# Kernel optimization log

Measured on AMD Instinct MI355X. Metric: run time of the kernel, lower is better.

## Reference

```python
import jax, jax.numpy as jnp
import numpy as np
from math import sqrt

LOCAL_WINDOW = 32
STRIDE = 64


def _sparse_mask(L):
    # L_Q == L_K path of DozerAttention:
    #  - local window: diagonals at offsets 0..local_window//2 (both signs)
    #  - strided: diagonals at offsets 0, stride+1, 2*(stride+1), ... (both signs)
    i = jnp.arange(L)[:, None]
    j = jnp.arange(L)[None, :]
    d = jnp.abs(i - j)
    local = d <= (LOCAL_WINDOW // 2)
    strided = (d % (STRIDE + 1)) == 0
    return (local | strided).astype(jnp.float32)  # [L, L]


def setup_inputs() -> dict:
    key = jax.random.key(0)
    B, L, H, D = 2, 2048, 8, 64
    kq, kk, kv = jax.random.split(key, 3)
    queries = jax.random.normal(kq, (B, L, H, D), dtype=jnp.float32)
    keys = jax.random.normal(kk, (B, L, H, D), dtype=jnp.float32)
    values = jax.random.normal(kv, (B, L, H, D), dtype=jnp.float32)
    # TriangularCausalMask: True above the diagonal -> masked with -inf
    causal = jnp.triu(jnp.ones((L, L), dtype=bool), k=1)
    attn_mask = jnp.broadcast_to(causal[None, None], (B, 1, L, L))
    return {"queries": queries, "keys": keys, "values": values, "attn_mask": attn_mask}


def reference(queries, keys, values, attn_mask):
    B, L, H, D = queries.shape
    scale = 1.0 / sqrt(D)
    sm = _sparse_mask(L)  # [L, L]
    # Original fills a zero-initialized dense score tensor only at selected key
    # columns per query row; equivalent to dense QK^T elementwise-masked by sm
    # (non-selected entries stay exactly 0, NOT -inf -- faithful quirk).
    scores = jnp.einsum('blhe,bshe->bhls', queries, keys) * sm  # [B,H,L,L]
    scores = jnp.where(attn_mask, -jnp.inf, scores)
    A = jax.nn.softmax(scale * scores, axis=-1)  # dropout p=0.0 in this config
    V = jnp.einsum('bhls,bshd->blhd', A, values)  # [B,L,H,D]
    return V
```

## Files before the change

kernel.cpp:

```cpp
#include <hip/hip_runtime.h>
#include <hip/hip_bf16.h>

#define B_ 2
#define L_ 2048
#define H_ 8
#define D_ 64
#define SP_ 65
#define NC_ 128
#define NL2_ 8
#define RS_ 512

typedef __attribute__((ext_vector_type(8))) short bf16x8;
typedef __attribute__((ext_vector_type(16))) float f32x16;

static __device__ inline short f2bf(float x) {
    return __builtin_bit_cast(short, __float2bfloat16(x));
}

static __device__ inline bf16x8 ld8_bf16(const float* __restrict__ p) {
    float4 a = *(const float4*)p;
    float4 b = *(const float4*)(p + 4);
    bf16x8 r;
    r[0]=f2bf(a.x); r[1]=f2bf(a.y); r[2]=f2bf(a.z); r[3]=f2bf(a.w);
    r[4]=f2bf(b.x); r[5]=f2bf(b.y); r[6]=f2bf(b.z); r[7]=f2bf(b.w);
    return r;
}

static __device__ inline bf16x8 ones_frag() {
    bf16x8 r;
    short o = f2bf(1.f);
    #pragma unroll
    for (int t = 0; t < 8; ++t) r[t] = o;
    return r;
}

__global__ __launch_bounds__(256) void partials_k(const float* __restrict__ q,
                                                  const float* __restrict__ kk,
                                                  const float* __restrict__ v,
                                                  float* __restrict__ csum1,
                                                  float* __restrict__ csum2,
                                                  float* __restrict__ pA,
                                                  float* __restrict__ zA,
                                                  float* __restrict__ pB,
                                                  float* __restrict__ zB) {
    __shared__ float Pw[4][32][68];
    int wib  = threadIdx.x >> 6;
    int lane = threadIdx.x & 63;
    int half = lane >> 5, ln = lane & 31;
    int u = blockIdx.x * 4 + wib;

    if (u < 1024) {
        int bh = u >> 6;
        int T  = (u & 63) << 5;
        int h = bh & 7, b = bh >> 3;
        const size_t base = (size_t)b * L_ * RS_ + (size_t)h * D_;

        bf16x8 bv0[4], bv1[4];
        #pragma unroll
        for (int kb = 0; kb < 4; ++kb) {
            int k0 = kb * 16 + half * 8;
            #pragma unroll
            for (int jj = 0; jj < 8; ++jj) {
                int jr = T - 16 + k0 + jj;
                jr = jr < 0 ? 0 : (jr > L_ - 1 ? L_ - 1 : jr);
                const float* vr = v + base + (size_t)jr * RS_;
                bv0[kb][jj] = f2bf(vr[ln]);
                bv1[kb][jj] = f2bf(vr[32 + ln]);
            }
        }

        const float* qrow = q + base + (size_t)(T + ln) * RS_;
        bf16x8 aq[4];
        #pragma unroll
        for (int kb = 0; kb < 4; ++kb) aq[kb] = ld8_bf16(qrow + kb * 16 + half * 8);

        int j0 = T - 16 + ln; j0 = j0 < 0 ? 0 : j0;
        int j1 = T + 16 + ln; j1 = j1 > L_ - 1 ? L_ - 1 : j1;
        const float* kr0 = kk + base + (size_t)j0 * RS_;
        const float* kr1 = kk + base + (size_t)j1 * RS_;
        f32x16 acc0 = {}; f32x16 acc1 = {};
        #pragma unroll
        for (int kb = 0; kb < 4; ++kb) {
            bf16x8 b0 = ld8_bf16(kr0 + kb * 16 + half * 8);
            bf16x8 b1 = ld8_bf16(kr1 + kb * 16 + half * 8);
            acc0 = __builtin_amdgcn_mfma_f32_32x32x16_bf16(aq[kb], b0, acc0, 0, 0, 0);
            acc1 = __builtin_amdgcn_mfma_f32_32x32x16_bf16(aq[kb], b1, acc1, 0, 0, 0);
        }

        #pragma unroll
        for (int r = 0; r < 16; ++r) {
            int m = (r & 3) + 8 * (r >> 2) + 4 * half;
            bool a0 = (ln >= m) && (ln <= m + 16) && (T - 16 + ln >= 0);
            float w0 = a0 ? (__expf(0.125f * acc0[r]) - 1.f) : 0.f;
            if ((m < 16) && (ln >= 16) && (ln <= m + 16)) w0 += 1.f;
            bool a1 = (ln <= m - 16);
            float w1 = a1 ? (__expf(0.125f * acc1[r]) - 1.f) : 0.f;
            if ((m >= 16) && (ln <= m - 16)) w1 += 1.f;
            Pw[wib][m][ln]      = w0;
            Pw[wib][m][32 + ln] = w1;
        }
        __syncthreads();

        f32x16 p0 = {}; f32x16 p1 = {}; f32x16 po = {};
        bf16x8 ones = ones_frag();
        #pragma unroll
        for (int kb = 0; kb < 4; ++kb) {
            int k0 = kb * 16 + half * 8;
            const float* pr = &Pw[wib][ln][k0];
            float4 x = *(const float4*)pr;
            float4 y = *(const float4*)(pr + 4);
            bf16x8 ap;
            ap[0]=f2bf(x.x); ap[1]=f2bf(x.y); ap[2]=f2bf(x.z); ap[3]=f2bf(x.w);
            ap[4]=f2bf(y.x); ap[5]=f2bf(y.y); ap[6]=f2bf(y.z); ap[7]=f2bf(y.w);
            p0 = __builtin_amdgcn_mfma_f32_32x32x16_bf16(ap, bv0[kb], p0, 0, 0, 0);
            p1 = __builtin_amdgcn_mfma_f32_32x32x16_bf16(ap, bv1[kb], p1, 0, 0, 0);
            po = __builtin_amdgcn_mfma_f32_32x32x16_bf16(ap, ones,    po, 0, 0, 0);
        }

        float* pAr = pA + (size_t)bh * L_ * D_;
        float* zAr = zA + (size_t)bh * L_;
        #pragma unroll
        for (int r = 0; r < 16; ++r) {
            int m = (r & 3) + 8 * (r >> 2) + 4 * half;
            int i = T + m;
            pAr[(size_t)i * D_ + ln]      = p0[r];
            pAr[(size_t)i * D_ + 32 + ln] = p1[r];
            if (ln == 0) zAr[i] = po[r] - (float)((m & 15) + 1);
        }
    } else if (u < 2064) {
        int us = u - 1024;
        int bh = us / SP_;
        int r  = us % SP_;
        int h = bh & 7, b = bh >> 3;
        const size_t base = (size_t)b * L_ * RS_ + (size_t)h * D_;

        bf16x8 bv0[2], bv1[2];
        #pragma unroll
        for (int kb = 0; kb < 2; ++kb) {
            int k0 = kb * 16 + half * 8;
            #pragma unroll
            for (int jj = 0; jj < 8; ++jj) {
                int lv = r + SP_ * (k0 + jj);
                lv = lv > L_ - 1 ? L_ - 1 : lv;
                const float* vr = v + base + (size_t)lv * RS_;
                bv0[kb][jj] = f2bf(vr[ln]);
                bv1[kb][jj] = f2bf(vr[32 + ln]);
            }
        }

        int lq = r + SP_ * ln;
        int lqc = lq > L_ - 1 ? L_ - 1 : lq;
        const float* qrow = q  + base + (size_t)lqc * RS_;
        const float* krow = kk + base + (size_t)lqc * RS_;
        f32x16 acc = {};
        #pragma unroll
        for (int kb = 0; kb < 4; ++kb) {
            bf16x8 a  = ld8_bf16(qrow + kb * 16 + half * 8);
            bf16x8 bb = ld8_bf16(krow + kb * 16 + half * 8);
            acc = __builtin_amdgcn_mfma_f32_32x32x16_bf16(a, bb, acc, 0, 0, 0);
        }
        #pragma unroll
        for (int rg = 0; rg < 16; ++rg) {
            int m = (rg & 3) + 8 * (rg >> 2) + 4 * half;
            bool act = (ln < m) && (r + SP_ * m < L_);
            Pw[wib][m][ln] = act ? (__expf(0.125f * acc[rg]) - 1.f) : 0.f;
        }
        __syncthreads();

        f32x16 p0 = {}; f32x16 p1 = {}; f32x16 po = {};
        bf16x8 ones = ones_frag();
        #pragma unroll
        for (int kb = 0; kb < 2; ++kb) {
            int k0 = kb * 16 + half * 8;
            const float* pr = &Pw[wib][ln][k0];
            float4 x = *(const float4*)pr;
            float4 y = *(const float4*)(pr + 4);
            bf16x8 ap;
            ap[0]=f2bf(x.x); ap[1]=f2bf(x.y); ap[2]=f2bf(x.z); ap[3]=f2bf(x.w);
            ap[4]=f2bf(y.x); ap[5]=f2bf(y.y); ap[6]=f2bf(y.z); ap[7]=f2bf(y.w);
            p0 = __builtin_amdgcn_mfma_f32_32x32x16_bf16(ap, bv0[kb], p0, 0, 0, 0);
            p1 = __builtin_amdgcn_mfma_f32_32x32x16_bf16(ap, bv1[kb], p1, 0, 0, 0);
            po = __builtin_amdgcn_mfma_f32_32x32x16_bf16(ap, ones,    po, 0, 0, 0);
        }
        float* pBr = pB + (size_t)bh * L_ * D_;
        float* zBr = zB + (size_t)bh * L_;
        #pragma unroll
        for (int rg = 0; rg < 16; ++rg) {
            int m = (rg & 3) + 8 * (rg >> 2) + 4 * half;
            int l = r + SP_ * m;
            if (l < L_) {
                pBr[(size_t)l * D_ + ln]      = p0[rg];
                pBr[(size_t)l * D_ + 32 + ln] = p1[rg];
                if (ln == 0) zBr[l] = po[rg];
            }
        }
    } else if (u < 4112) {
        int uc = u - 2064;
        int c = uc & (NC_ - 1);
        int bh = uc >> 7;
        int h = bh & 7, b = bh >> 3;
        const float* vb = v + (size_t)(b * L_ + c * 16) * RS_ + h * D_ + lane;
        float s = 0.f;
        #pragma unroll
        for (int l = 0; l < 16; ++l) s += vb[l * RS_];
        csum1[(size_t)uc * D_ + lane] = s;
    } else {
        int uc = u - 4112;
        int c2 = uc & 7;
        int bh = uc >> 3;
        int h = bh & 7, b = bh >> 3;
        const float* vb = v + (size_t)(b * L_ + c2 * 256) * RS_ + h * D_ + lane;
        float s0 = 0.f, s1 = 0.f, s2 = 0.f, s3 = 0.f;
        for (int l = 0; l < 256; l += 4) {
            s0 += vb[(l + 0) * RS_]; s1 += vb[(l + 1) * RS_];
            s2 += vb[(l + 2) * RS_]; s3 += vb[(l + 3) * RS_];
        }
        csum2[(size_t)uc * D_ + lane] = (s0 + s1) + (s2 + s3);
    }
}

__global__ __launch_bounds__(256) void combine_k(const float* __restrict__ csum1,
                                                 const float* __restrict__ csum2,
                                                 const float* __restrict__ pA,
                                                 const float* __restrict__ zA,
                                                 const float* __restrict__ pB,
                                                 const float* __restrict__ zB,
                                                 float* __restrict__ out) {
    int wib  = threadIdx.x >> 6;
    int lane = threadIdx.x & 63;
    int u = blockIdx.x * 4 + wib;
    int bh = u >> 7;
    int g  = u & 127;
    int i0 = g << 4;
    int h = bh & 7, b = bh >> 3;

    int c2 = i0 >> 8;
    const float* cs2 = csum2 + (size_t)bh * NL2_ * D_;
    const float* cs1 = csum1 + (size_t)bh * NC_ * D_;
    float pr = 0.f;
    for (int cc = 0; cc < c2; ++cc)        pr += cs2[cc * D_ + lane];
    for (int cc = c2 << 4; cc < g; ++cc)   pr += cs1[cc * D_ + lane];

    const float* pAr = pA + (size_t)bh * L_ * D_;
    const float* pBr = pB + (size_t)bh * L_ * D_;
    const float* zAr = zA + (size_t)bh * L_;
    const float* zBr = zB + (size_t)bh * L_;
    const size_t obase = (size_t)b * L_ * RS_ + (size_t)h * D_;

    #pragma unroll
    for (int r = 0; r < 16; ++r) {
        int i = i0 + r;
        float num = pAr[(size_t)i * D_ + lane] + pBr[(size_t)i * D_ + lane] + pr;
        float inv = 1.f / (zAr[i] + zBr[i] + (float)(i + 1));
        out[obase + (size_t)i * RS_ + lane] = num * inv;
    }
}

extern "C" void kernel_launch(void* const* d_in, const int* in_sizes, int n_in,
                              void* d_out, int out_size, void* d_ws, size_t ws_size,
                              hipStream_t stream) {
    const float* q = (const float*)d_in[0];
    const float* k = (const float*)d_in[1];
    const float* v = (const float*)d_in[2];
    float* out = (float*)d_out;

    float* csum1 = (float*)d_ws;
    float* csum2 = csum1 + (size_t)B_ * H_ * NC_ * D_;
    float* pA    = csum2 + (size_t)B_ * H_ * NL2_ * D_;
    float* zA    = pA    + (size_t)B_ * H_ * L_ * D_;
    float* pB    = zA    + (size_t)B_ * H_ * L_;
    float* zB    = pB    + (size_t)B_ * H_ * L_ * D_;

    partials_k<<<1060, 256, 0, stream>>>(q, k, v, csum1, csum2, pA, zA, pB, zB);
    combine_k<<<512, 256, 0, stream>>>(csum1, csum2, pA, zA, pB, zB, out);
}
```

Measured before the change: 116.4 us.

## Split local-band tiles across wave pairs, drop coarse chunk sums, halve combine rows

```diff
diff --git a/kernel.cpp b/kernel.cpp
--- a/kernel.cpp
+++ b/kernel.cpp
@@ -7,7 +7,6 @@
 #define D_ 64
 #define SP_ 65
 #define NC_ 128
-#define NL2_ 8
 #define RS_ 512
 
 typedef __attribute__((ext_vector_type(8))) short bf16x8;
@@ -38,34 +37,35 @@
                                                   const float* __restrict__ kk,
                                                   const float* __restrict__ v,
                                                   float* __restrict__ csum1,
-                                                  float* __restrict__ csum2,
                                                   float* __restrict__ pA,
                                                   float* __restrict__ zA,
                                                   float* __restrict__ pB,
                                                   float* __restrict__ zB) {
-    __shared__ float Pw[4][32][68];
+    __shared__ float LDS[4608];
     int wib  = threadIdx.x >> 6;
     int lane = threadIdx.x & 63;
     int half = lane >> 5, ln = lane & 31;
-    int u = blockIdx.x * 4 + wib;
-
-    if (u < 1024) {
-        int bh = u >> 6;
-        int T  = (u & 63) << 5;
+    int blk  = blockIdx.x;
+
+    if (blk < 512) {
+        int tb = wib >> 1;
+        int hf = wib & 1;
+        int team = blk * 2 + tb;
+        int bh = team >> 6;
+        int T  = (team & 63) << 5;
         int h = bh & 7, b = bh >> 3;
         const size_t base = (size_t)b * L_ * RS_ + (size_t)h * D_;
-
-        bf16x8 bv0[4], bv1[4];
-        #pragma unroll
-        for (int kb = 0; kb < 4; ++kb) {
-            int k0 = kb * 16 + half * 8;
+        float* Pw = LDS + tb * 2176;
+        int d0 = 32 * hf;
+
+        bf16x8 bv[4];
+        #pragma unroll
+        for (int kb = 0; kb < 4; ++kb) {
             #pragma unroll
             for (int jj = 0; jj < 8; ++jj) {
-                int jr = T - 16 + k0 + jj;
+                int jr = T - 16 + kb * 16 + half * 8 + jj;
                 jr = jr < 0 ? 0 : (jr > L_ - 1 ? L_ - 1 : jr);
-                const float* vr = v + base + (size_t)jr * RS_;
-                bv0[kb][jj] = f2bf(vr[ln]);
-                bv1[kb][jj] = f2bf(vr[32 + ln]);
+                bv[kb][jj] = f2bf(v[base + (size_t)jr * RS_ + d0 + ln]);
             }
         }
 
@@ -74,47 +74,47 @@
         #pragma unroll
         for (int kb = 0; kb < 4; ++kb) aq[kb] = ld8_bf16(qrow + kb * 16 + half * 8);
 
-        int j0 = T - 16 + ln; j0 = j0 < 0 ? 0 : j0;
-        int j1 = T + 16 + ln; j1 = j1 > L_ - 1 ? L_ - 1 : j1;
-        const float* kr0 = kk + base + (size_t)j0 * RS_;
-        const float* kr1 = kk + base + (size_t)j1 * RS_;
-        f32x16 acc0 = {}; f32x16 acc1 = {};
-        #pragma unroll
-        for (int kb = 0; kb < 4; ++kb) {
-            bf16x8 b0 = ld8_bf16(kr0 + kb * 16 + half * 8);
-            bf16x8 b1 = ld8_bf16(kr1 + kb * 16 + half * 8);
-            acc0 = __builtin_amdgcn_mfma_f32_32x32x16_bf16(aq[kb], b0, acc0, 0, 0, 0);
-            acc1 = __builtin_amdgcn_mfma_f32_32x32x16_bf16(aq[kb], b1, acc1, 0, 0, 0);
+        int j = T - 16 + 32 * hf + ln;
+        j = j < 0 ? 0 : (j > L_ - 1 ? L_ - 1 : j);
+        const float* krow = kk + base + (size_t)j * RS_;
+        f32x16 acc = {};
+        #pragma unroll
+        for (int kb = 0; kb < 4; ++kb) {
+            bf16x8 kf = ld8_bf16(krow + kb * 16 + half * 8);
+            acc = __builtin_amdgcn_mfma_f32_32x32x16_bf16(aq[kb], kf, acc, 0, 0, 0);
         }
 
         #pragma unroll
         for (int r = 0; r < 16; ++r) {
             int m = (r & 3) + 8 * (r >> 2) + 4 * half;
-            bool a0 = (ln >= m) && (ln <= m + 16) && (T - 16 + ln >= 0);
-            float w0 = a0 ? (__expf(0.125f * acc0[r]) - 1.f) : 0.f;
-            if ((m < 16) && (ln >= 16) && (ln <= m + 16)) w0 += 1.f;
-            bool a1 = (ln <= m - 16);
-            float w1 = a1 ? (__expf(0.125f * acc1[r]) - 1.f) : 0.f;
-            if ((m >= 16) && (ln <= m - 16)) w1 += 1.f;
-            Pw[wib][m][ln]      = w0;
-            Pw[wib][m][32 + ln] = w1;
+            float w;
+            if (hf == 0) {
+                bool act = (ln >= m) && (ln <= m + 16) && (T - 16 + ln >= 0);
+                w = act ? (__expf(0.125f * acc[r]) - 1.f) : 0.f;
+                if ((m < 16) && (ln >= 16) && (ln <= m + 16)) w += 1.f;
+            } else {
+                bool act = (ln <= m - 16);
+                w = act ? (__expf(0.125f * acc[r]) - 1.f) : 0.f;
+                if ((m >= 16) && (ln <= m - 16)) w += 1.f;
+            }
+            Pw[m * 68 + d0 + ln] = w;
         }
         __syncthreads();
 
-        f32x16 p0 = {}; f32x16 p1 = {}; f32x16 po = {};
+        f32x16 p = {}; f32x16 po = {};
         bf16x8 ones = ones_frag();
         #pragma unroll
         for (int kb = 0; kb < 4; ++kb) {
             int k0 = kb * 16 + half * 8;
-            const float* pr = &Pw[wib][ln][k0];
+            const float* pr = &Pw[ln * 68 + k0];
             float4 x = *(const float4*)pr;
             float4 y = *(const float4*)(pr + 4);
             bf16x8 ap;
             ap[0]=f2bf(x.x); ap[1]=f2bf(x.y); ap[2]=f2bf(x.z); ap[3]=f2bf(x.w);
             ap[4]=f2bf(y.x); ap[5]=f2bf(y.y); ap[6]=f2bf(y.z); ap[7]=f2bf(y.w);
-            p0 = __builtin_amdgcn_mfma_f32_32x32x16_bf16(ap, bv0[kb], p0, 0, 0, 0);
-            p1 = __builtin_amdgcn_mfma_f32_32x32x16_bf16(ap, bv1[kb], p1, 0, 0, 0);
-            po = __builtin_amdgcn_mfma_f32_32x32x16_bf16(ap, ones,    po, 0, 0, 0);
+            p = __builtin_amdgcn_mfma_f32_32x32x16_bf16(ap, bv[kb], p, 0, 0, 0);
+            if (hf == 0)
+                po = __builtin_amdgcn_mfma_f32_32x32x16_bf16(ap, ones, po, 0, 0, 0);
         }
 
         float* pAr = pA + (size_t)bh * L_ * D_;
@@ -123,16 +123,17 @@
         for (int r = 0; r < 16; ++r) {
             int m = (r & 3) + 8 * (r >> 2) + 4 * half;
             int i = T + m;
-            pAr[(size_t)i * D_ + ln]      = p0[r];
-            pAr[(size_t)i * D_ + 32 + ln] = p1[r];
-            if (ln == 0) zAr[i] = po[r] - (float)((m & 15) + 1);
-        }
-    } else if (u < 2064) {
-        int us = u - 1024;
+            pAr[(size_t)i * D_ + d0 + ln] = p[r];
+            if (hf == 0 && ln == 0)
+                zAr[i] = po[r] - (float)((m & 15) + 1);
+        }
+    } else if (blk < 772) {
+        int us = (blk - 512) * 4 + wib;
         int bh = us / SP_;
         int r  = us % SP_;
         int h = bh & 7, b = bh >> 3;
         const size_t base = (size_t)b * L_ * RS_ + (size_t)h * D_;
+        float* Pw = LDS + wib * 1152;
 
         bf16x8 bv0[2], bv1[2];
         #pragma unroll
@@ -163,7 +164,7 @@
         for (int rg = 0; rg < 16; ++rg) {
             int m = (rg & 3) + 8 * (rg >> 2) + 4 * half;
             bool act = (ln < m) && (r + SP_ * m < L_);
-            Pw[wib][m][ln] = act ? (__expf(0.125f * acc[rg]) - 1.f) : 0.f;
+            Pw[m * 36 + ln] = act ? (__expf(0.125f * acc[rg]) - 1.f) : 0.f;
         }
         __syncthreads();
 
@@ -172,7 +173,7 @@
         #pragma unroll
         for (int kb = 0; kb < 2; ++kb) {
             int k0 = kb * 16 + half * 8;
-            const float* pr = &Pw[wib][ln][k0];
+            const float* pr = &Pw[ln * 36 + k0];
             float4 x = *(const float4*)pr;
             float4 y = *(const float4*)(pr + 4);
             bf16x8 ap;
@@ -194,8 +195,8 @@
                 if (ln == 0) zBr[l] = po[rg];
             }
         }
-    } else if (u < 4112) {
-        int uc = u - 2064;
+    } else {
+        int uc = (blk - 772) * 4 + wib;
         int c = uc & (NC_ - 1);
         int bh = uc >> 7;
         int h = bh & 7, b = bh >> 3;
@@ -204,23 +205,10 @@
         #pragma unroll
         for (int l = 0; l < 16; ++l) s += vb[l * RS_];
         csum1[(size_t)uc * D_ + lane] = s;
-    } else {
-        int uc = u - 4112;
-        int c2 = uc & 7;
-        int bh = uc >> 3;
-        int h = bh & 7, b = bh >> 3;
-        const float* vb = v + (size_t)(b * L_ + c2 * 256) * RS_ + h * D_ + lane;
-        float s0 = 0.f, s1 = 0.f, s2 = 0.f, s3 = 0.f;
-        for (int l = 0; l < 256; l += 4) {
-            s0 += vb[(l + 0) * RS_]; s1 += vb[(l + 1) * RS_];
-            s2 += vb[(l + 2) * RS_]; s3 += vb[(l + 3) * RS_];
-        }
-        csum2[(size_t)uc * D_ + lane] = (s0 + s1) + (s2 + s3);
     }
 }
 
 __global__ __launch_bounds__(256) void combine_k(const float* __restrict__ csum1,
-                                                 const float* __restrict__ csum2,
                                                  const float* __restrict__ pA,
                                                  const float* __restrict__ zA,
                                                  const float* __restrict__ pB,
@@ -229,17 +217,21 @@
     int wib  = threadIdx.x >> 6;
     int lane = threadIdx.x & 63;
     int u = blockIdx.x * 4 + wib;
-    int bh = u >> 7;
-    int g  = u & 127;
-    int i0 = g << 4;
+    int bh = u >> 8;
+    int g  = u & 255;
+    int i0 = g << 3;
+    int c1 = i0 >> 4;
     int h = bh & 7, b = bh >> 3;
 
-    int c2 = i0 >> 8;
-    const float* cs2 = csum2 + (size_t)bh * NL2_ * D_;
-    const float* cs1 = csum1 + (size_t)bh * NC_ * D_;
-    float pr = 0.f;
-    for (int cc = 0; cc < c2; ++cc)        pr += cs2[cc * D_ + lane];
-    for (int cc = c2 << 4; cc < g; ++cc)   pr += cs1[cc * D_ + lane];
+    const float* cs1 = csum1 + (size_t)bh * NC_ * D_ + lane;
+    float s0 = 0.f, s1 = 0.f, s2 = 0.f, s3 = 0.f;
+    int cc = 0;
+    for (; cc + 4 <= c1; cc += 4) {
+        s0 += cs1[(cc + 0) * D_]; s1 += cs1[(cc + 1) * D_];
+        s2 += cs1[(cc + 2) * D_]; s3 += cs1[(cc + 3) * D_];
+    }
+    for (; cc < c1; ++cc) s0 += cs1[cc * D_];
+    float pr = (s0 + s1) + (s2 + s3);
 
     const float* pAr = pA + (size_t)bh * L_ * D_;
     const float* pBr = pB + (size_t)bh * L_ * D_;
@@ -248,7 +240,7 @@
     const size_t obase = (size_t)b * L_ * RS_ + (size_t)h * D_;
 
     #pragma unroll
-    for (int r = 0; r < 16; ++r) {
+    for (int r = 0; r < 8; ++r) {
         int i = i0 + r;
         float num = pAr[(size_t)i * D_ + lane] + pBr[(size_t)i * D_ + lane] + pr;
         float inv = 1.f / (zAr[i] + zBr[i] + (float)(i + 1));
@@ -265,12 +257,11 @@
     float* out = (float*)d_out;
 
     float* csum1 = (float*)d_ws;
-    float* csum2 = csum1 + (size_t)B_ * H_ * NC_ * D_;
-    float* pA    = csum2 + (size_t)B_ * H_ * NL2_ * D_;
+    float* pA    = csum1 + (size_t)B_ * H_ * NC_ * D_;
     float* zA    = pA    + (size_t)B_ * H_ * L_ * D_;
     float* pB    = zA    + (size_t)B_ * H_ * L_;
     float* zB    = pB    + (size_t)B_ * H_ * L_ * D_;
 
-    partials_k<<<1060, 256, 0, stream>>>(q, k, v, csum1, csum2, pA, zA, pB, zB);
-    combine_k<<<512, 256, 0, stream>>>(csum1, csum2, pA, zA, pB, zB, out);
-}
+    partials_k<<<1284, 256, 0, stream>>>(q, k, v, csum1, pA, zA, pB, zB);
+    combine_k<<<1024, 256, 0, stream>>>(csum1, pA, zA, pB, zB, out);
+}
```

Measured after the change: 112.0 us. 3.8% less time.
